# Kernel tuning notes

Hardware: AMD Instinct MI355X
Metric: run time of the kernel (lower is better)

## Reference

```python
import jax, jax.numpy as jnp
import numpy as np

N = 50000      # nodes
E = 800000     # edges (avg degree 16)
IN, HID, OUT = 256, 128, 64
K, ALPHA = 4, 0.0  # APPNPConv(k=4, alpha=0.0)


def setup_inputs() -> dict:
    key = jax.random.key(0)
    ks = jax.random.split(key, 5)
    features = jax.random.normal(ks[0], (N, IN), jnp.float32)
    src = jax.random.randint(ks[1], (E,), 0, N, jnp.int32)
    dst = jax.random.randint(ks[2], (E,), 0, N, jnp.int32)
    W1 = jax.random.normal(ks[3], (IN, HID), jnp.float32) / np.float32(np.sqrt(IN))
    b1 = jnp.zeros((HID,), jnp.float32)
    W3 = jax.random.normal(ks[4], (HID, OUT), jnp.float32) / np.float32(np.sqrt(HID))
    b3 = jnp.zeros((OUT,), jnp.float32)
    return dict(features=features, src=src, dst=dst, W1=W1, b1=b1, W3=W3, b3=b3)


def _sym_norms(src, dst, n):
    # D_out^{-1/2} for source side, D_in^{-1/2} for destination side (DGL norm='both')
    ones = jnp.ones((src.shape[0],), jnp.float32)
    deg_out = jax.ops.segment_sum(ones, src, num_segments=n)
    deg_in = jax.ops.segment_sum(ones, dst, num_segments=n)
    return jnp.clip(deg_out, 1.0) ** -0.5, jnp.clip(deg_in, 1.0) ** -0.5


def _prop(x, src, dst, norm_src, norm_dst):
    # x: [N, D]. Symmetric-normalized SpMM: D_in^{-1/2} A D_out^{-1/2} x
    msg = (x * norm_src[:, None])[src]                       # [E, D] gather
    agg = jax.ops.segment_sum(msg, dst, num_segments=x.shape[0])  # [N, D] scatter-add
    return agg * norm_dst[:, None]


def reference(features, src, dst, W1, b1, W3, b3):
    ns, nd = _sym_norms(src, dst, N)
    # GraphConv 1 (weight-first since in_dim > hidden_dim; math identical either way)
    h = _prop(features @ W1, src, dst, ns, nd) + b1
    # dropout is identity in eval mode (training=False)
    # APPNPConv: k=4 power-iteration steps with teleport alpha=0.0
    h0 = h
    for _ in range(K):
        h = (1.0 - ALPHA) * _prop(h, src, dst, ns, nd) + ALPHA * h0
    # GraphConv 3
    out = _prop(h @ W3, src, dst, ns, nd) + b3
    return out
```

## Files before the change

### kernel.cpp

```cpp
#include <hip/hip_runtime.h>
#include <math.h>

#define N_NODES 50000
#define N_EDGES 800000
#define DIN 256
#define DHID 128
#define DOUT 64
#define CSTRIDE 64
#define ZROW N_NODES
#define HBLOCKS 256
#define HCHUNK (N_EDGES / HBLOCKS)
#define HWORDS (N_NODES / 4)
#define SLICE ((size_t)(N_NODES + 1) * 16)
#define NGROUPS (N_NODES / 4)


__global__ void k_sent(unsigned int* __restrict__ csr32) {
    int i = blockIdx.x * 256 + threadIdx.x;
    unsigned int v = (unsigned int)ZROW | ((unsigned int)ZROW << 16);
    uint2 o; o.x = v; o.y = v;
    ((uint2*)csr32)[i] = o;
}

__global__ void k_hist(const int* __restrict__ idx, unsigned int* __restrict__ partials) {
    __shared__ unsigned int h[HWORDS];
    int t = threadIdx.x;
    for (int w = t; w < HWORDS; w += 256) h[w] = 0u;
    __syncthreads();
    int base = blockIdx.x * HCHUNK;
    for (int i = t; i < HCHUNK; i += 256) {
        int s = idx[base + i];
        atomicAdd(&h[s >> 2], 1u << ((s & 3) << 3));
    }
    __syncthreads();
    unsigned int* outp = partials + (size_t)blockIdx.x * HWORDS;
    for (int w = t; w < HWORDS; w += 256) outp[w] = h[w];
}

__global__ void k_hpre(const unsigned int* __restrict__ pS,
                       const unsigned int* __restrict__ pD,
                       unsigned int* __restrict__ prefix,
                       int* __restrict__ deg_in,
                       float* __restrict__ ns, float* __restrict__ nd,
                       float* __restrict__ cc) {
    int wid = blockIdx.x * 256 + threadIdx.x;
    if (wid >= HWORDS) return;
    unsigned int o0 = 0, o1 = 0, o2 = 0, o3 = 0;
#pragma unroll 4
    for (int b = 0; b < HBLOCKS; ++b) {
        unsigned int w = pS[(size_t)b * HWORDS + wid];
        o0 += w & 0xffu; o1 += (w >> 8) & 0xffu;
        o2 += (w >> 16) & 0xffu; o3 += w >> 24;
    }
    unsigned int run = 0;
    for (int b = 0; b < HBLOCKS; ++b) {
        unsigned int w = pD[(size_t)b * HWORDS + wid];
        prefix[(size_t)b * HWORDS + wid] = run;
        run += w;
    }
    unsigned int i0 = run & 0xffu, i1 = (run >> 8) & 0xffu;
    unsigned int i2 = (run >> 16) & 0xffu, i3 = run >> 24;
    int4 di; di.x = (int)i0; di.y = (int)i1; di.z = (int)i2; di.w = (int)i3;
    *(int4*)(deg_in + (wid << 2)) = di;

    unsigned int dov[4] = {o0, o1, o2, o3};
    unsigned int div_[4] = {i0, i1, i2, i3};
    float4 vns, vnd, vcc;
    float* pns = &vns.x; float* pnd = &vnd.x; float* pcc = &vcc.x;
#pragma unroll
    for (int q = 0; q < 4; ++q) {
        unsigned int a = dov[q] < 1u ? 1u : dov[q];
        unsigned int b = div_[q] < 1u ? 1u : div_[q];
        float fa = 1.0f / sqrtf((float)a);
        float fb = 1.0f / sqrtf((float)b);
        pns[q] = fa; pnd[q] = fb; pcc[q] = fa * fb;
    }
    *(float4*)(ns + (wid << 2)) = vns;
    *(float4*)(nd + (wid << 2)) = vnd;
    *(float4*)(cc + (wid << 2)) = vcc;
}

__global__ void k_fill(const int* __restrict__ src, const int* __restrict__ dst,
                       const unsigned int* __restrict__ prefix,
                       unsigned short* __restrict__ csr) {
    __shared__ unsigned int h[HWORDS];
    int t = threadIdx.x;
    const unsigned int* prow = prefix + (size_t)blockIdx.x * HWORDS;
    for (int w = t; w < HWORDS; w += 256) h[w] = prow[w];
    __syncthreads();
    int base = blockIdx.x * HCHUNK;
    for (int i = t; i < HCHUNK; i += 256) {
        int s = src[base + i], d = dst[base + i];
        int sh = (d & 3) << 3;
        unsigned int old = atomicAdd(&h[d >> 2], 1u << sh);
        int slot = (int)((old >> sh) & 0xffu);
        csr[(d << 6) + slot] = (unsigned short)s;
    }
}


__global__ void k_weights(const float* __restrict__ W1, const float* __restrict__ b1,
                          const float* __restrict__ W3,
                          float* __restrict__ W13, float* __restrict__ bb,
                          float* __restrict__ Y0, float* __restrict__ Y1) {
    if (blockIdx.x == 65) {
        int t = threadIdx.x;
        if (t < 64) {
            int qq = t >> 4, c2 = t & 15;
            Y0[(size_t)qq * SLICE + ((size_t)ZROW << 4) + c2] = 0.f;
            Y1[(size_t)qq * SLICE + ((size_t)ZROW << 4) + c2] = 0.f;
        }
        return;
    }
    if (blockIdx.x == 64) {
        int j = threadIdx.x;
        if (j < DOUT) {
            float s = 0.f;
            for (int k = 0; k < DHID; ++k) s += b1[k] * W3[k * DOUT + j];
            bb[j] = s;
        }
        return;
    }
    int idx = blockIdx.x * 256 + threadIdx.x;
    int i = idx >> 6, j = idx & 63;
    float s = 0.f;
    for (int k = 0; k < DHID; ++k) s += W1[i * DHID + k] * W3[k * DOUT + j];
    W13[idx] = s;
}


__global__ void k_gemm(const float* __restrict__ X, const float* __restrict__ W13,
                       const float* __restrict__ ns, float* __restrict__ Y) {
    __shared__ float As[16][68];
    __shared__ float Bs[16][64];
    int tid = threadIdx.x;
    int tx = tid & 15, ty = tid >> 4;
    int row0 = blockIdx.x * 64;
    float acc[4][4];
#pragma unroll
    for (int i = 0; i < 4; ++i)
#pragma unroll
        for (int j = 0; j < 4; ++j) acc[i][j] = 0.f;

    int lr = tid >> 2;
    int lk = (tid & 3) << 2;
    int arow = row0 + lr;
    if (arow > N_NODES - 1) arow = N_NODES - 1;

    for (int k0 = 0; k0 < DIN; k0 += 16) {
        float4 a = *(const float4*)(X + (size_t)arow * DIN + k0 + lk);
        As[lk + 0][lr] = a.x; As[lk + 1][lr] = a.y;
        As[lk + 2][lr] = a.z; As[lk + 3][lr] = a.w;
        float4 b = *(const float4*)(W13 + (size_t)(k0 + (tid >> 4)) * DOUT + ((tid & 15) << 2));
        *(float4*)&Bs[tid >> 4][(tid & 15) << 2] = b;
        __syncthreads();
#pragma unroll
        for (int k = 0; k < 16; ++k) {
            float4 av = *(const float4*)&As[k][ty << 2];
            float4 bv = *(const float4*)&Bs[k][tx << 2];
            float ar[4] = {av.x, av.y, av.z, av.w};
            float br[4] = {bv.x, bv.y, bv.z, bv.w};
#pragma unroll
            for (int i = 0; i < 4; ++i)
#pragma unroll
                for (int j = 0; j < 4; ++j) acc[i][j] += ar[i] * br[j];
        }
        __syncthreads();
    }
    int qq = tx >> 2;
    int co = (tx & 3) << 2;
#pragma unroll
    for (int i = 0; i < 4; ++i) {
        int row = row0 + (ty << 2) + i;
        if (row < N_NODES) {
            float nsr = ns[row];
            float4 o;
            o.x = acc[i][0] * nsr; o.y = acc[i][1] * nsr;
            o.z = acc[i][2] * nsr; o.w = acc[i][3] * nsr;
            *(float4*)(Y + (size_t)qq * SLICE + ((size_t)row << 4) + co) = o;
        }
    }
}


template <int MODE>
__launch_bounds__(256, 8)
__global__ void k_spmm(const float* __restrict__ xs, float* __restrict__ ys,
                       const unsigned short* __restrict__ csr,
                       const int* __restrict__ cnt,
                       const float* __restrict__ cc, const float* __restrict__ ns,
                       const float* __restrict__ nd,
                       const float* __restrict__ bb, const float* __restrict__ b3) {
    __shared__ unsigned short rows[4][4][64];
    int wid  = threadIdx.x >> 6;
    int lane = threadIdx.x & 63;
    int q    = (blockIdx.x & 7) >> 1;
    int half = blockIdx.x & 1;
    int g    = (blockIdx.x >> 3) * 8 + wid * 2 + half;
    if (g >= NGROUPS) return;
    int node0 = g << 2;

    int nn = lane >> 4, sl = lane & 15;
    const unsigned short* crow = csr + ((size_t)(node0 + nn) << 6) + sl;
    unsigned short r0 = crow[0], r1 = crow[16], r2 = crow[32], r3 = crow[48];
    unsigned short* myrow = &rows[wid][nn][0];
    myrow[sl] = r0; myrow[sl + 16] = r1; myrow[sl + 32] = r2; myrow[sl + 48] = r3;

    int n0u = __builtin_amdgcn_readfirstlane(node0);
    int m = cnt[n0u];
    int t1 = cnt[n0u + 1]; if (t1 > m) m = t1;
    int t2 = cnt[n0u + 2]; if (t2 > m) m = t2;
    int t3 = cnt[n0u + 3]; if (t3 > m) m = t3;
    m = (m + 7) & ~7;

    int n = lane >> 4, e = (lane >> 2) & 3, c4 = lane & 3;
    const unsigned short* rd = &rows[wid][n][e];
    const float* xq = xs + (size_t)q * SLICE + (c4 << 2);

    float ax = 0.f, ay = 0.f, az = 0.f, aw = 0.f;
    for (int j = 0; j < m; j += 8) {
        int s0 = rd[j];
        int s1 = rd[j + 4];
        const float4 t0v = *(const float4*)(xq + ((size_t)s0 << 4));
        const float4 t1v = *(const float4*)(xq + ((size_t)s1 << 4));
        ax += t0v.x; ay += t0v.y; az += t0v.z; aw += t0v.w;
        ax += t1v.x; ay += t1v.y; az += t1v.z; aw += t1v.w;
    }
    ax += __shfl_xor(ax, 4);  ay += __shfl_xor(ay, 4);
    az += __shfl_xor(az, 4);  aw += __shfl_xor(aw, 4);
    ax += __shfl_xor(ax, 8);  ay += __shfl_xor(ay, 8);
    az += __shfl_xor(az, 8);  aw += __shfl_xor(aw, 8);

    int nodeL = node0 + n;
    int colq  = (q << 4) + (c4 << 2);
    float4 r;
    if (MODE == 0) {
        float cv = cc[nodeL], nv = ns[nodeL];
        float4 bv = *(const float4*)(bb + colq);
        r.x = cv * ax + nv * bv.x; r.y = cv * ay + nv * bv.y;
        r.z = cv * az + nv * bv.z; r.w = cv * aw + nv * bv.w;
    } else if (MODE == 1) {
        float cv = cc[nodeL];
        r.x = cv * ax; r.y = cv * ay; r.z = cv * az; r.w = cv * aw;
    } else {
        float dv = nd[nodeL];
        float4 bv = *(const float4*)(b3 + colq);
        r.x = dv * ax + bv.x; r.y = dv * ay + bv.y;
        r.z = dv * az + bv.z; r.w = dv * aw + bv.w;
    }
    if (e == 0) {
        if (MODE == 2)
            *(float4*)(ys + ((size_t)nodeL << 6) + colq) = r;
        else
            *(float4*)(ys + (size_t)q * SLICE + ((size_t)nodeL << 4) + (c4 << 2)) = r;
    }
}


extern "C" void kernel_launch(void* const* d_in, const int* in_sizes, int n_in,
                              void* d_out, int out_size, void* d_ws, size_t ws_size,
                              hipStream_t stream) {
    const float* X   = (const float*)d_in[0];
    const int*   src = (const int*)d_in[1];
    const int*   dst = (const int*)d_in[2];
    const float* W1  = (const float*)d_in[3];
    const float* b1  = (const float*)d_in[4];
    const float* W3  = (const float*)d_in[5];
    const float* b3  = (const float*)d_in[6];
    float* out = (float*)d_out;

    char* ws = (char*)d_ws;
    size_t off = 0;
    auto alloc = [&](size_t bytes) -> void* {
        void* p = ws + off;
        off = (off + bytes + 255) & ~(size_t)255;
        return p;
    };
    const size_t BIGSZ = SLICE * 4 * 4;
    char* bufA = (char*)alloc(BIGSZ);
    char* bufB = (char*)alloc(BIGSZ);
    int*            deg_in  = (int*)alloc((size_t)N_NODES * 4);
    unsigned short* csr     = (unsigned short*)alloc((size_t)N_NODES * CSTRIDE * 2);
    float*          ns      = (float*)alloc((size_t)N_NODES * 4);
    float*          nd      = (float*)alloc((size_t)N_NODES * 4);
    float*          cc      = (float*)alloc((size_t)N_NODES * 4);
    float*          W13     = (float*)alloc((size_t)DIN * DOUT * 4);
    float*          bb      = (float*)alloc(DOUT * 4);

    unsigned int* pS   = (unsigned int*)bufA;
    unsigned int* pD   = (unsigned int*)bufB;
    unsigned int* pref = (unsigned int*)bufA;
    float*        Y0   = (float*)bufB;
    float*        Y1   = (float*)bufA;

    const int hblk = (HWORDS + 255) / 256;
    const int sblk = 1563 * 8;

    k_sent<<<(N_EDGES / 256), 256, 0, stream>>>((unsigned int*)csr);
    k_hist<<<HBLOCKS, 256, 0, stream>>>(src, pS);
    k_hist<<<HBLOCKS, 256, 0, stream>>>(dst, pD);
    k_hpre<<<hblk, 256, 0, stream>>>(pS, pD, pref, deg_in, ns, nd, cc);
    k_fill<<<HBLOCKS, 256, 0, stream>>>(src, dst, pref, csr);

    k_weights<<<66, 256, 0, stream>>>(W1, b1, W3, W13, bb, Y0, Y1);

    k_gemm<<<(N_NODES + 63) / 64, 256, 0, stream>>>(X, W13, ns, Y0);

    k_spmm<0><<<sblk, 256, 0, stream>>>(Y0, Y1, csr, deg_in, cc, ns, nd, bb, b3);
    k_spmm<1><<<sblk, 256, 0, stream>>>(Y1, Y0, csr, deg_in, cc, ns, nd, bb, b3);
    k_spmm<1><<<sblk, 256, 0, stream>>>(Y0, Y1, csr, deg_in, cc, ns, nd, bb, b3);
    k_spmm<1><<<sblk, 256, 0, stream>>>(Y1, Y0, csr, deg_in, cc, ns, nd, bb, b3);
    k_spmm<1><<<sblk, 256, 0, stream>>>(Y0, Y1, csr, deg_in, cc, ns, nd, bb, b3);
    k_spmm<2><<<sblk, 256, 0, stream>>>(Y1, out, csr, deg_in, cc, ns, nd, bb, b3);
}
```

Measured before the change: 326.2 us.

## Reorder nodes by in-degree descending and fuse setup kernels into one launch

Nodes are sorted into in-degree buckets in descending order with a histogram, scan and scatter, and the CSR, features and per-node norms are stored in that permuted order. Each group of four nodes in the SpMM then has similar degrees, so the loop bound comes from one degree read and less work is wasted on padding. The gather loop is specialised into fixed unrolled cases, the CSR row is loaded as uint2, and the sentinel, histogram and weight-fold kernels are merged into one launch. The cost is extra preprocessing kernels and permutation indirection in the fill, GEMM store and final output write. The gathers also lose whatever locality the original node order had.

```diff
diff --git a/kernel.cpp b/kernel.cpp
--- a/kernel.cpp
+++ b/kernel.cpp
@@ -13,28 +13,66 @@
 #define HWORDS (N_NODES / 4)
 #define SLICE ((size_t)(N_NODES + 1) * 16)
 #define NGROUPS (N_NODES / 4)
-
-
-__global__ void k_sent(unsigned int* __restrict__ csr32) {
-    int i = blockIdx.x * 256 + threadIdx.x;
-    unsigned int v = (unsigned int)ZROW | ((unsigned int)ZROW << 16);
-    uint2 o; o.x = v; o.y = v;
-    ((uint2*)csr32)[i] = o;
-}
-
-__global__ void k_hist(const int* __restrict__ idx, unsigned int* __restrict__ partials) {
+#define PBLOCKS 49
+
+#define SB_SENT 3125
+#define SB_HS (SB_SENT + HBLOCKS)
+#define SB_HD (SB_HS + HBLOCKS)
+#define SB_TOT (SB_HD + 66)
+
+__global__ void k_setup(const int* __restrict__ src, const int* __restrict__ dst,
+                        unsigned int* __restrict__ pS, unsigned int* __restrict__ pD,
+                        unsigned int* __restrict__ csr32,
+                        const float* __restrict__ W1, const float* __restrict__ b1,
+                        const float* __restrict__ W3,
+                        float* __restrict__ W13, float* __restrict__ bb,
+                        float* __restrict__ Y0, float* __restrict__ Y1) {
     __shared__ unsigned int h[HWORDS];
-    int t = threadIdx.x;
-    for (int w = t; w < HWORDS; w += 256) h[w] = 0u;
-    __syncthreads();
-    int base = blockIdx.x * HCHUNK;
-    for (int i = t; i < HCHUNK; i += 256) {
-        int s = idx[base + i];
-        atomicAdd(&h[s >> 2], 1u << ((s & 3) << 3));
-    }
-    __syncthreads();
-    unsigned int* outp = partials + (size_t)blockIdx.x * HWORDS;
-    for (int w = t; w < HWORDS; w += 256) outp[w] = h[w];
+    int bx = blockIdx.x, t = threadIdx.x;
+    if (bx < SB_SENT) {
+        unsigned int v = (unsigned int)ZROW | ((unsigned int)ZROW << 16);
+        uint2 o; o.x = v; o.y = v;
+        ((uint2*)csr32)[bx * 256 + t] = o;
+        return;
+    }
+    if (bx < SB_HD) {
+        const int* idx = (bx < SB_HS) ? src : dst;
+        unsigned int* outp = (bx < SB_HS) ? pS : pD;
+        int hb = bx - ((bx < SB_HS) ? SB_SENT : SB_HS);
+        for (int w = t; w < HWORDS; w += 256) h[w] = 0u;
+        __syncthreads();
+        int base = hb * HCHUNK;
+        for (int i = t; i < HCHUNK; i += 256) {
+            int s = idx[base + i];
+            atomicAdd(&h[s >> 2], 1u << ((s & 3) << 3));
+        }
+        __syncthreads();
+        outp += (size_t)hb * HWORDS;
+        for (int w = t; w < HWORDS; w += 256) outp[w] = h[w];
+        return;
+    }
+    int vb = bx - SB_HD;
+    if (vb == 65) {
+        if (t < 64) {
+            int qq = t >> 4, c2 = t & 15;
+            Y0[(size_t)qq * SLICE + ((size_t)ZROW << 4) + c2] = 0.f;
+            Y1[(size_t)qq * SLICE + ((size_t)ZROW << 4) + c2] = 0.f;
+        }
+        return;
+    }
+    if (vb == 64) {
+        if (t < DOUT) {
+            float s = 0.f;
+            for (int k = 0; k < DHID; ++k) s += b1[k] * W3[k * DOUT + t];
+            bb[t] = s;
+        }
+        return;
+    }
+    int idx2 = vb * 256 + t;
+    int i = idx2 >> 6, j = idx2 & 63;
+    float s = 0.f;
+    for (int k = 0; k < DHID; ++k) s += W1[i * DHID + k] * W3[k * DOUT + j];
+    W13[idx2] = s;
 }
 
 __global__ void k_hpre(const unsigned int* __restrict__ pS,
@@ -42,46 +80,102 @@
                        unsigned int* __restrict__ prefix,
                        int* __restrict__ deg_in,
                        float* __restrict__ ns, float* __restrict__ nd,
-                       float* __restrict__ cc) {
-    int wid = blockIdx.x * 256 + threadIdx.x;
-    if (wid >= HWORDS) return;
-    unsigned int o0 = 0, o1 = 0, o2 = 0, o3 = 0;
+                       float* __restrict__ cc, int* __restrict__ dparts) {
+    __shared__ int lh[65];
+    int t = threadIdx.x;
+    if (t < 65) lh[t] = 0;
+    __syncthreads();
+    int wid = blockIdx.x * 256 + t;
+    if (wid < HWORDS) {
+        unsigned int o0 = 0, o1 = 0, o2 = 0, o3 = 0;
 #pragma unroll 4
-    for (int b = 0; b < HBLOCKS; ++b) {
-        unsigned int w = pS[(size_t)b * HWORDS + wid];
-        o0 += w & 0xffu; o1 += (w >> 8) & 0xffu;
-        o2 += (w >> 16) & 0xffu; o3 += w >> 24;
-    }
-    unsigned int run = 0;
-    for (int b = 0; b < HBLOCKS; ++b) {
-        unsigned int w = pD[(size_t)b * HWORDS + wid];
-        prefix[(size_t)b * HWORDS + wid] = run;
-        run += w;
-    }
-    unsigned int i0 = run & 0xffu, i1 = (run >> 8) & 0xffu;
-    unsigned int i2 = (run >> 16) & 0xffu, i3 = run >> 24;
-    int4 di; di.x = (int)i0; di.y = (int)i1; di.z = (int)i2; di.w = (int)i3;
-    *(int4*)(deg_in + (wid << 2)) = di;
-
-    unsigned int dov[4] = {o0, o1, o2, o3};
-    unsigned int div_[4] = {i0, i1, i2, i3};
-    float4 vns, vnd, vcc;
-    float* pns = &vns.x; float* pnd = &vnd.x; float* pcc = &vcc.x;
-#pragma unroll
-    for (int q = 0; q < 4; ++q) {
-        unsigned int a = dov[q] < 1u ? 1u : dov[q];
-        unsigned int b = div_[q] < 1u ? 1u : div_[q];
-        float fa = 1.0f / sqrtf((float)a);
-        float fb = 1.0f / sqrtf((float)b);
-        pns[q] = fa; pnd[q] = fb; pcc[q] = fa * fb;
-    }
-    *(float4*)(ns + (wid << 2)) = vns;
-    *(float4*)(nd + (wid << 2)) = vnd;
-    *(float4*)(cc + (wid << 2)) = vcc;
+        for (int b = 0; b < HBLOCKS; ++b) {
+            unsigned int w = pS[(size_t)b * HWORDS + wid];
+            o0 += w & 0xffu; o1 += (w >> 8) & 0xffu;
+            o2 += (w >> 16) & 0xffu; o3 += w >> 24;
+        }
+        unsigned int run = 0;
+        for (int b = 0; b < HBLOCKS; ++b) {
+            unsigned int w = pD[(size_t)b * HWORDS + wid];
+            prefix[(size_t)b * HWORDS + wid] = run;
+            run += w;
+        }
+        unsigned int i0 = run & 0xffu, i1 = (run >> 8) & 0xffu;
+        unsigned int i2 = (run >> 16) & 0xffu, i3 = run >> 24;
+        int4 di; di.x = (int)i0; di.y = (int)i1; di.z = (int)i2; di.w = (int)i3;
+        *(int4*)(deg_in + (wid << 2)) = di;
+
+        unsigned int dov[4] = {o0, o1, o2, o3};
+        unsigned int div_[4] = {i0, i1, i2, i3};
+        float4 vns, vnd, vcc;
+        float* pns = &vns.x; float* pnd = &vnd.x; float* pcc = &vcc.x;
+#pragma unroll
+        for (int q = 0; q < 4; ++q) {
+            int bin = (int)div_[q]; if (bin > 64) bin = 64;
+            atomicAdd(&lh[bin], 1);
+            unsigned int a = dov[q] < 1u ? 1u : dov[q];
+            unsigned int b = div_[q] < 1u ? 1u : div_[q];
+            float fa = 1.0f / sqrtf((float)a);
+            float fb = 1.0f / sqrtf((float)b);
+            pns[q] = fa; pnd[q] = fb; pcc[q] = fa * fb;
+        }
+        *(float4*)(ns + (wid << 2)) = vns;
+        *(float4*)(nd + (wid << 2)) = vnd;
+        *(float4*)(cc + (wid << 2)) = vcc;
+    }
+    __syncthreads();
+    if (t < 65) dparts[blockIdx.x * 65 + t] = lh[t];
+}
+
+__global__ void k_dscan(const int* __restrict__ dparts, int* __restrict__ offs) {
+    __shared__ int colsum[65], binbase[65];
+    int t = threadIdx.x;
+    if (t < 65) {
+        int s = 0;
+        for (int b = 0; b < PBLOCKS; ++b) s += dparts[b * 65 + t];
+        colsum[t] = s;
+    }
+    __syncthreads();
+    if (t == 0) {
+        int run = 0;
+        for (int k = 64; k >= 0; --k) { binbase[k] = run; run += colsum[k]; }
+    }
+    __syncthreads();
+    if (t < 65) {
+        int run = binbase[t];
+        for (int b = 0; b < PBLOCKS; ++b) { offs[b * 65 + t] = run; run += dparts[b * 65 + t]; }
+    }
+}
+
+__global__ void k_dscatter(const int* __restrict__ deg_in, const int* __restrict__ offs,
+                           const float* __restrict__ cc, const float* __restrict__ ns,
+                           const float* __restrict__ nd,
+                           int* __restrict__ perm, int* __restrict__ inv,
+                           int* __restrict__ degP, float* __restrict__ ccP,
+                           float* __restrict__ nsP, float* __restrict__ ndP) {
+    __shared__ int off[65];
+    int t = threadIdx.x;
+    if (t < 65) off[t] = offs[blockIdx.x * 65 + t];
+    __syncthreads();
+    int wid = blockIdx.x * 256 + t;
+    if (wid < HWORDS) {
+        int4 d4 = *(const int4*)(deg_in + (wid << 2));
+        int dd[4] = {d4.x, d4.y, d4.z, d4.w};
+#pragma unroll
+        for (int k = 0; k < 4; ++k) {
+            int node = (wid << 2) + k;
+            int bin = dd[k] > 64 ? 64 : dd[k];
+            int slot = atomicAdd(&off[bin], 1);
+            perm[slot] = node; inv[node] = slot;
+            degP[slot] = dd[k];
+            ccP[slot] = cc[node]; nsP[slot] = ns[node]; ndP[slot] = nd[node];
+        }
+    }
 }
 
 __global__ void k_fill(const int* __restrict__ src, const int* __restrict__ dst,
                        const unsigned int* __restrict__ prefix,
+                       const int* __restrict__ inv,
                        unsigned short* __restrict__ csr) {
     __shared__ unsigned int h[HWORDS];
     int t = threadIdx.x;
@@ -94,43 +188,13 @@
         int sh = (d & 3) << 3;
         unsigned int old = atomicAdd(&h[d >> 2], 1u << sh);
         int slot = (int)((old >> sh) & 0xffu);
-        csr[(d << 6) + slot] = (unsigned short)s;
-    }
-}
-
-
-__global__ void k_weights(const float* __restrict__ W1, const float* __restrict__ b1,
-                          const float* __restrict__ W3,
-                          float* __restrict__ W13, float* __restrict__ bb,
-                          float* __restrict__ Y0, float* __restrict__ Y1) {
-    if (blockIdx.x == 65) {
-        int t = threadIdx.x;
-        if (t < 64) {
-            int qq = t >> 4, c2 = t & 15;
-            Y0[(size_t)qq * SLICE + ((size_t)ZROW << 4) + c2] = 0.f;
-            Y1[(size_t)qq * SLICE + ((size_t)ZROW << 4) + c2] = 0.f;
-        }
-        return;
-    }
-    if (blockIdx.x == 64) {
-        int j = threadIdx.x;
-        if (j < DOUT) {
-            float s = 0.f;
-            for (int k = 0; k < DHID; ++k) s += b1[k] * W3[k * DOUT + j];
-            bb[j] = s;
-        }
-        return;
-    }
-    int idx = blockIdx.x * 256 + threadIdx.x;
-    int i = idx >> 6, j = idx & 63;
-    float s = 0.f;
-    for (int k = 0; k < DHID; ++k) s += W1[i * DHID + k] * W3[k * DOUT + j];
-    W13[idx] = s;
-}
-
+        csr[((size_t)inv[d] << 6) + slot] = (unsigned short)inv[s];
+    }
+}
 
 __global__ void k_gemm(const float* __restrict__ X, const float* __restrict__ W13,
-                       const float* __restrict__ ns, float* __restrict__ Y) {
+                       const float* __restrict__ ns, const int* __restrict__ inv,
+                       float* __restrict__ Y) {
     __shared__ float As[16][68];
     __shared__ float Bs[16][64];
     int tid = threadIdx.x;
@@ -174,10 +238,11 @@
         int row = row0 + (ty << 2) + i;
         if (row < N_NODES) {
             float nsr = ns[row];
+            int prow = inv[row];
             float4 o;
             o.x = acc[i][0] * nsr; o.y = acc[i][1] * nsr;
             o.z = acc[i][2] * nsr; o.w = acc[i][3] * nsr;
-            *(float4*)(Y + (size_t)qq * SLICE + ((size_t)row << 4) + co) = o;
+            *(float4*)(Y + (size_t)qq * SLICE + ((size_t)prow << 4) + co) = o;
         }
     }
 }
@@ -187,10 +252,11 @@
 __launch_bounds__(256, 8)
 __global__ void k_spmm(const float* __restrict__ xs, float* __restrict__ ys,
                        const unsigned short* __restrict__ csr,
-                       const int* __restrict__ cnt,
-                       const float* __restrict__ cc, const float* __restrict__ ns,
-                       const float* __restrict__ nd,
-                       const float* __restrict__ bb, const float* __restrict__ b3) {
+                       const int* __restrict__ degP,
+                       const float* __restrict__ ccP, const float* __restrict__ nsP,
+                       const float* __restrict__ ndP,
+                       const float* __restrict__ bb, const float* __restrict__ b3,
+                       const int* __restrict__ perm) {
     __shared__ unsigned short rows[4][4][64];
     int wid  = threadIdx.x >> 6;
     int lane = threadIdx.x & 63;
@@ -201,31 +267,42 @@
     int node0 = g << 2;
 
     int nn = lane >> 4, sl = lane & 15;
-    const unsigned short* crow = csr + ((size_t)(node0 + nn) << 6) + sl;
-    unsigned short r0 = crow[0], r1 = crow[16], r2 = crow[32], r3 = crow[48];
-    unsigned short* myrow = &rows[wid][nn][0];
-    myrow[sl] = r0; myrow[sl + 16] = r1; myrow[sl + 32] = r2; myrow[sl + 48] = r3;
+    const uint2* crow = (const uint2*)(csr + ((size_t)(node0 + nn) << 6)) + sl;
+    uint2 rv = *crow;
+    *(uint2*)(&rows[wid][nn][sl << 2]) = rv;
 
     int n0u = __builtin_amdgcn_readfirstlane(node0);
-    int m = cnt[n0u];
-    int t1 = cnt[n0u + 1]; if (t1 > m) m = t1;
-    int t2 = cnt[n0u + 2]; if (t2 > m) m = t2;
-    int t3 = cnt[n0u + 3]; if (t3 > m) m = t3;
-    m = (m + 7) & ~7;
+    int m = (degP[n0u] + 7) & ~7;
 
     int n = lane >> 4, e = (lane >> 2) & 3, c4 = lane & 3;
     const unsigned short* rd = &rows[wid][n][e];
     const float* xq = xs + (size_t)q * SLICE + (c4 << 2);
 
     float ax = 0.f, ay = 0.f, az = 0.f, aw = 0.f;
-    for (int j = 0; j < m; j += 8) {
-        int s0 = rd[j];
-        int s1 = rd[j + 4];
-        const float4 t0v = *(const float4*)(xq + ((size_t)s0 << 4));
-        const float4 t1v = *(const float4*)(xq + ((size_t)s1 << 4));
-        ax += t0v.x; ay += t0v.y; az += t0v.z; aw += t0v.w;
-        ax += t1v.x; ay += t1v.y; az += t1v.z; aw += t1v.w;
-    }
+#define LDV(T) const float4 v##T = *(const float4*)(xq + ((size_t)rd[4 * (T)] << 4))
+#define ACCV(T) ax += v##T.x; ay += v##T.y; az += v##T.z; aw += v##T.w
+    if (m <= 8) {
+        LDV(0); LDV(1);
+        ACCV(0); ACCV(1);
+    } else if (m <= 16) {
+        LDV(0); LDV(1); LDV(2); LDV(3);
+        ACCV(0); ACCV(1); ACCV(2); ACCV(3);
+    } else if (m <= 24) {
+        LDV(0); LDV(1); LDV(2); LDV(3); LDV(4); LDV(5);
+        ACCV(0); ACCV(1); ACCV(2); ACCV(3); ACCV(4); ACCV(5);
+    } else if (m <= 32) {
+        LDV(0); LDV(1); LDV(2); LDV(3); LDV(4); LDV(5); LDV(6); LDV(7);
+        ACCV(0); ACCV(1); ACCV(2); ACCV(3); ACCV(4); ACCV(5); ACCV(6); ACCV(7);
+    } else {
+        for (int j = 0; j < m; j += 8) {
+            const float4 a = *(const float4*)(xq + ((size_t)rd[j] << 4));
+            const float4 b = *(const float4*)(xq + ((size_t)rd[j + 4] << 4));
+            ax += a.x; ay += a.y; az += a.z; aw += a.w;
+            ax += b.x; ay += b.y; az += b.z; aw += b.w;
+        }
+    }
+#undef LDV
+#undef ACCV
     ax += __shfl_xor(ax, 4);  ay += __shfl_xor(ay, 4);
     az += __shfl_xor(az, 4);  aw += __shfl_xor(aw, 4);
     ax += __shfl_xor(ax, 8);  ay += __shfl_xor(ay, 8);
@@ -235,24 +312,26 @@
     int colq  = (q << 4) + (c4 << 2);
     float4 r;
     if (MODE == 0) {
-        float cv = cc[nodeL], nv = ns[nodeL];
+        float cv = ccP[nodeL], nv = nsP[nodeL];
         float4 bv = *(const float4*)(bb + colq);
         r.x = cv * ax + nv * bv.x; r.y = cv * ay + nv * bv.y;
         r.z = cv * az + nv * bv.z; r.w = cv * aw + nv * bv.w;
     } else if (MODE == 1) {
-        float cv = cc[nodeL];
+        float cv = ccP[nodeL];
         r.x = cv * ax; r.y = cv * ay; r.z = cv * az; r.w = cv * aw;
     } else {
-        float dv = nd[nodeL];
+        float dv = ndP[nodeL];
         float4 bv = *(const float4*)(b3 + colq);
         r.x = dv * ax + bv.x; r.y = dv * ay + bv.y;
         r.z = dv * az + bv.z; r.w = dv * aw + bv.w;
     }
     if (e == 0) {
-        if (MODE == 2)
-            *(float4*)(ys + ((size_t)nodeL << 6) + colq) = r;
-        else
+        if (MODE == 2) {
+            int orow = perm[nodeL];
+            *(float4*)(ys + ((size_t)orow << 6) + colq) = r;
+        } else {
             *(float4*)(ys + (size_t)q * SLICE + ((size_t)nodeL << 4) + (c4 << 2)) = r;
+        }
     }
 }
 
@@ -276,40 +355,43 @@
         off = (off + bytes + 255) & ~(size_t)255;
         return p;
     };
-    const size_t BIGSZ = SLICE * 4 * 4;
-    char* bufA = (char*)alloc(BIGSZ);
-    char* bufB = (char*)alloc(BIGSZ);
-    int*            deg_in  = (int*)alloc((size_t)N_NODES * 4);
-    unsigned short* csr     = (unsigned short*)alloc((size_t)N_NODES * CSTRIDE * 2);
-    float*          ns      = (float*)alloc((size_t)N_NODES * 4);
-    float*          nd      = (float*)alloc((size_t)N_NODES * 4);
-    float*          cc      = (float*)alloc((size_t)N_NODES * 4);
-    float*          W13     = (float*)alloc((size_t)DIN * DOUT * 4);
-    float*          bb      = (float*)alloc(DOUT * 4);
-
-    unsigned int* pS   = (unsigned int*)bufA;
-    unsigned int* pD   = (unsigned int*)bufB;
-    unsigned int* pref = (unsigned int*)bufA;
-    float*        Y0   = (float*)bufB;
-    float*        Y1   = (float*)bufA;
-
-    const int hblk = (HWORDS + 255) / 256;
+    unsigned int*   pS     = (unsigned int*)alloc((size_t)HBLOCKS * HWORDS * 4);
+    unsigned int*   pD     = (unsigned int*)alloc((size_t)HBLOCKS * HWORDS * 4);
+    unsigned int*   pref   = (unsigned int*)alloc((size_t)HBLOCKS * HWORDS * 4);
+    float*          Y0     = (float*)alloc(SLICE * 4 * 4);
+    float*          Y1     = (float*)alloc(SLICE * 4 * 4);
+    unsigned short* csr    = (unsigned short*)alloc((size_t)N_NODES * CSTRIDE * 2);
+    int*            deg_in = (int*)alloc((size_t)N_NODES * 4);
+    float*          ns     = (float*)alloc((size_t)N_NODES * 4);
+    float*          nd     = (float*)alloc((size_t)N_NODES * 4);
+    float*          cc     = (float*)alloc((size_t)N_NODES * 4);
+    int*            perm   = (int*)alloc((size_t)N_NODES * 4);
+    int*            inv    = (int*)alloc((size_t)N_NODES * 4);
+    int*            degP   = (int*)alloc((size_t)N_NODES * 4);
+    float*          ccP    = (float*)alloc((size_t)N_NODES * 4);
+    float*          nsP    = (float*)alloc((size_t)N_NODES * 4);
+    float*          ndP    = (float*)alloc((size_t)N_NODES * 4);
+    int*            dparts = (int*)alloc((size_t)PBLOCKS * 65 * 4);
+    int*            offs   = (int*)alloc((size_t)PBLOCKS * 65 * 4);
+    float*          W13    = (float*)alloc((size_t)DIN * DOUT * 4);
+    float*          bb     = (float*)alloc(DOUT * 4);
+
     const int sblk = 1563 * 8;
 
-    k_sent<<<(N_EDGES / 256), 256, 0, stream>>>((unsigned int*)csr);
-    k_hist<<<HBLOCKS, 256, 0, stream>>>(src, pS);
-    k_hist<<<HBLOCKS, 256, 0, stream>>>(dst, pD);
-    k_hpre<<<hblk, 256, 0, stream>>>(pS, pD, pref, deg_in, ns, nd, cc);
-    k_fill<<<HBLOCKS, 256, 0, stream>>>(src, dst, pref, csr);
-
-    k_weights<<<66, 256, 0, stream>>>(W1, b1, W3, W13, bb, Y0, Y1);
-
-    k_gemm<<<(N_NODES + 63) / 64, 256, 0, stream>>>(X, W13, ns, Y0);
-
-    k_spmm<0><<<sblk, 256, 0, stream>>>(Y0, Y1, csr, deg_in, cc, ns, nd, bb, b3);
-    k_spmm<1><<<sblk, 256, 0, stream>>>(Y1, Y0, csr, deg_in, cc, ns, nd, bb, b3);
-    k_spmm<1><<<sblk, 256, 0, stream>>>(Y0, Y1, csr, deg_in, cc, ns, nd, bb, b3);
-    k_spmm<1><<<sblk, 256, 0, stream>>>(Y1, Y0, csr, deg_in, cc, ns, nd, bb, b3);
-    k_spmm<1><<<sblk, 256, 0, stream>>>(Y0, Y1, csr, deg_in, cc, ns, nd, bb, b3);
-    k_spmm<2><<<sblk, 256, 0, stream>>>(Y1, out, csr, deg_in, cc, ns, nd, bb, b3);
-}
+    k_setup<<<SB_TOT, 256, 0, stream>>>(src, dst, pS, pD, (unsigned int*)csr,
+                                        W1, b1, W3, W13, bb, Y0, Y1);
+    k_hpre<<<PBLOCKS, 256, 0, stream>>>(pS, pD, pref, deg_in, ns, nd, cc, dparts);
+    k_dscan<<<1, 256, 0, stream>>>(dparts, offs);
+    k_dscatter<<<PBLOCKS, 256, 0, stream>>>(deg_in, offs, cc, ns, nd,
+                                            perm, inv, degP, ccP, nsP, ndP);
+    k_fill<<<HBLOCKS, 256, 0, stream>>>(src, dst, pref, inv, csr);
+
+    k_gemm<<<(N_NODES + 63) / 64, 256, 0, stream>>>(X, W13, ns, inv, Y0);
+
+    k_spmm<0><<<sblk, 256, 0, stream>>>(Y0, Y1, csr, degP, ccP, nsP, ndP, bb, b3, perm);
+    k_spmm<1><<<sblk, 256, 0, stream>>>(Y1, Y0, csr, degP, ccP, nsP, ndP, bb, b3, perm);
+    k_spmm<1><<<sblk, 256, 0, stream>>>(Y0, Y1, csr, degP, ccP, nsP, ndP, bb, b3, perm);
+    k_spmm<1><<<sblk, 256, 0, stream>>>(Y1, Y0, csr, degP, ccP, nsP, ndP, bb, b3, perm);
+    k_spmm<1><<<sblk, 256, 0, stream>>>(Y0, Y1, csr, degP, ccP, nsP, ndP, bb, b3, perm);
+    k_spmm<2><<<sblk, 256, 0, stream>>>(Y1, out, csr, degP, ccP, nsP, ndP, bb, b3, perm);
+}
```

Result: faster. 315.3 us (-3.3%).
